# Optimization experiments

Hardware: AMD Instinct MI355X
Metric: run time of the kernel (lower is better)

## Reference

```python
import jax, jax.numpy as jnp
import numpy as np

N_NODES = 10000
N_EDGES = 320000
OBS_DIM = 30
ACT_DIM = 4
HID = 128


def setup_inputs() -> dict:
    key = jax.random.key(0)
    ks = jax.random.split(key, 16)

    def lin(k, fan_in, fan_out):
        s = 1.0 / np.sqrt(fan_in)
        kw, kb = jax.random.split(k)
        w = jax.random.uniform(kw, (fan_in, fan_out), jnp.float32, -s, s)
        b = jax.random.uniform(kb, (fan_out,), jnp.float32, -s, s)
        return w, b

    obs = jax.random.normal(ks[0], (N_NODES, OBS_DIM), jnp.float32)
    action = jax.random.normal(ks[1], (N_NODES, ACT_DIM), jnp.float32)
    edge_index = jax.random.randint(ks[2], (2, N_EDGES), 0, N_NODES, jnp.int64)

    w_g1, b_g1 = lin(ks[3], OBS_DIM + ACT_DIM, HID)
    w_g2, b_g2 = lin(ks[4], HID, HID)
    w_q1a, b_q1a = lin(ks[5], HID, HID)
    w_q1b, b_q1b = lin(ks[6], HID, 1)
    w_q2a, b_q2a = lin(ks[7], HID, HID)
    w_q2b, b_q2b = lin(ks[8], HID, 1)

    return dict(obs=obs, action=action, edge_index=edge_index,
                w_g1=w_g1, b_g1=b_g1, w_g2=w_g2, b_g2=b_g2,
                w_q1a=w_q1a, b_q1a=b_q1a, w_q1b=w_q1b, b_q1b=b_q1b,
                w_q2a=w_q2a, b_q2a=b_q2a, w_q2b=w_q2b, b_q2b=b_q2b)


def gcn_conv(x, w, b, src, dst, deg_inv_sqrt, n):
    xw = x @ w                                      # [N, Fout] small GEMM
    norm = deg_inv_sqrt[src] * deg_inv_sqrt[dst]    # [E'] edge norm
    msg = xw[src] * norm[:, None]                   # gather + scale, [E', Fout]
    out = jax.ops.segment_sum(msg, dst, num_segments=n)  # scatter-add
    return out + b


def reference(obs, action, edge_index,
              w_g1, b_g1, w_g2, b_g2,
              w_q1a, b_q1a, w_q1b, b_q1b,
              w_q2a, b_q2a, w_q2b, b_q2b):
    n = obs.shape[0]
    loops = jnp.arange(n, dtype=edge_index.dtype)
    src = jnp.concatenate([edge_index[0], loops])   # add self-loops
    dst = jnp.concatenate([edge_index[1], loops])

    deg = jnp.zeros((n,), jnp.float32).at[dst].add(1.0)
    deg_inv_sqrt = jnp.where(deg > 0, jax.lax.rsqrt(jnp.maximum(deg, 1.0)), 0.0)

    x = jnp.concatenate([obs, action], axis=1)
    x = jax.nn.relu(gcn_conv(x, w_g1, b_g1, src, dst, deg_inv_sqrt, n))
    x = jax.nn.relu(gcn_conv(x, w_g2, b_g2, src, dst, deg_inv_sqrt, n))

    q1 = jax.nn.relu(x @ w_q1a + b_q1a) @ w_q1b + b_q1b
    q2 = jax.nn.relu(x @ w_q2a + b_q2a) @ w_q2b + b_q2b
    return (q1, q2)
```

## Files before the change

### kernel.cpp

```cpp
#include <hip/hip_runtime.h>

#define N_NODES 10000
#define N_EDGES 320000
#define OBS_DIM 30
#define ACT_DIM 4
#define HID 128
#define ELL_W 128
#define SENT N_NODES


__global__ __launch_bounds__(256) void k_init(int* __restrict__ cnt,
                                              int* __restrict__ col,
                                              float* __restrict__ xpad,
                                              float* __restrict__ ph1,
                                              const float* __restrict__ obs,
                                              const float* __restrict__ act) {
    int i = blockIdx.x * 256 + threadIdx.x;
    if (i < N_NODES * ELL_W / 4)
        ((int4*)col)[i] = make_int4(SENT, SENT, SENT, SENT);
    if (i < (N_NODES + 1) * 16) {
        int row = i >> 4, sub = i & 15;
        float4 v = make_float4(0.f, 0.f, 0.f, 0.f);
        if (row < N_NODES) {
            float* vv = &v.x;
#pragma unroll
            for (int k = 0; k < 4; ++k) {
                int c = sub * 4 + k;
                if (c < OBS_DIM) vv[k] = obs[row * OBS_DIM + c];
                else if (c < OBS_DIM + ACT_DIM) vv[k] = act[row * ACT_DIM + (c - OBS_DIM)];
            }
        }
        ((float4*)xpad)[i] = v;
    }
    if (i <= N_NODES) cnt[i] = 0;
    if (i < HID / 4)
        ((float4*)(ph1 + (size_t)SENT * HID))[i] = make_float4(0.f, 0.f, 0.f, 0.f);
}


__global__ __launch_bounds__(256) void k_build(const int4* __restrict__ src4,
                                               const int4* __restrict__ dst4,
                                               int* __restrict__ cnt,
                                               int* __restrict__ col) {
    int i = blockIdx.x * 256 + threadIdx.x;
    if (i < N_EDGES / 4) {
        int4 s = src4[i];
        int4 d = dst4[i];
        int p;
        p = atomicAdd(&cnt[d.x], 1); col[(d.x << 7) + p] = s.x;
        p = atomicAdd(&cnt[d.y], 1); col[(d.y << 7) + p] = s.y;
        p = atomicAdd(&cnt[d.z], 1); col[(d.z << 7) + p] = s.z;
        p = atomicAdd(&cnt[d.w], 1); col[(d.w << 7) + p] = s.w;
    }
}


__global__ __launch_bounds__(512) void k_l1(const float4* __restrict__ x4,
                                            const int* __restrict__ cnt,
                                            const int* __restrict__ col,
                                            const float* __restrict__ W1,
                                            const float* __restrict__ b1,
                                            float* __restrict__ ph1) {
    __shared__ float w1s[34 * 128];
    __shared__ float zs[8][64];
    int t = threadIdx.x;
    {
        float4* wsp = (float4*)w1s;
        const float4* Wp = (const float4*)W1;
        for (int i = t; i < 1088; i += 512) wsp[i] = Wp[i];
    }
    __syncthreads();
    int wave = t >> 6, lane = t & 63, g = lane >> 4, sub = lane & 15;
    int node = blockIdx.x * 8 + wave;
    int deg = cnt[node];
    float di = rsqrtf((float)(deg + 1));
    const int* cp = col + (node << 7);
    float4 a = make_float4(0.f, 0.f, 0.f, 0.f);
    float4 b = make_float4(0.f, 0.f, 0.f, 0.f);
    if (g == 0) {
        float4 xv = x4[node * 16 + sub];
        a.x = di * xv.x; a.y = di * xv.y; a.z = di * xv.z; a.w = di * xv.w;
    }
    for (int e = 0; e < deg; e += 16) {
        int j0 = cp[e + g];
        int j1 = cp[e + 4 + g];
        int j2 = cp[e + 8 + g];
        int j3 = cp[e + 12 + g];
        float d0 = rsqrtf((float)(cnt[j0] + 1));
        float d1 = rsqrtf((float)(cnt[j1] + 1));
        float d2 = rsqrtf((float)(cnt[j2] + 1));
        float d3 = rsqrtf((float)(cnt[j3] + 1));
        float4 v0 = x4[j0 * 16 + sub];
        float4 v1 = x4[j1 * 16 + sub];
        float4 v2 = x4[j2 * 16 + sub];
        float4 v3 = x4[j3 * 16 + sub];
        a.x += d0 * v0.x + d1 * v1.x;
        a.y += d0 * v0.y + d1 * v1.y;
        a.z += d0 * v0.z + d1 * v1.z;
        a.w += d0 * v0.w + d1 * v1.w;
        b.x += d2 * v2.x + d3 * v3.x;
        b.y += d2 * v2.y + d3 * v3.y;
        b.z += d2 * v2.z + d3 * v3.z;
        b.w += d2 * v2.w + d3 * v3.w;
    }
    a.x += b.x; a.y += b.y; a.z += b.z; a.w += b.w;
    a.x += __shfl_xor(a.x, 16); a.x += __shfl_xor(a.x, 32);
    a.y += __shfl_xor(a.y, 16); a.y += __shfl_xor(a.y, 32);
    a.z += __shfl_xor(a.z, 16); a.z += __shfl_xor(a.z, 32);
    a.w += __shfl_xor(a.w, 16); a.w += __shfl_xor(a.w, 32);
    if (g == 0) {
        float4 z;
        z.x = di * a.x; z.y = di * a.y; z.z = di * a.z; z.w = di * a.w;
        *(float4*)&zs[wave][sub * 4] = z;
    }
    float h0 = b1[lane], h64 = b1[lane + 64];
#pragma unroll
    for (int k = 0; k < 34; ++k) {
        float zk = zs[wave][k];
        h0 += zk * w1s[k * 128 + lane];
        h64 += zk * w1s[k * 128 + 64 + lane];
    }
    ph1[node * HID + lane] = di * fmaxf(h0, 0.0f);
    ph1[node * HID + 64 + lane] = di * fmaxf(h64, 0.0f);
}


__global__ __launch_bounds__(256) void k_agg2(const float4* __restrict__ ph14,
                                              const int* __restrict__ cnt,
                                              const int* __restrict__ col,
                                              float4* __restrict__ sbuf) {
    int t = threadIdx.x;
    int wave = t >> 6, lane = t & 63, half = lane >> 5, sub = lane & 31;
    int node = blockIdx.x * 4 + wave;
    int deg = cnt[node];
    const int* cp = col + (node << 7);
    float4 a = make_float4(0.f, 0.f, 0.f, 0.f);
    float4 b = make_float4(0.f, 0.f, 0.f, 0.f);
    if (!half) a = ph14[node * 32 + sub];
    for (int e = 0; e < deg; e += 32) {
        int jj[16];
#pragma unroll
        for (int u = 0; u < 16; ++u) jj[u] = cp[e + 2 * u + half];
        float4 v[16];
#pragma unroll
        for (int u = 0; u < 16; ++u) v[u] = ph14[jj[u] * 32 + sub];
#pragma unroll
        for (int u = 0; u < 8; ++u) {
            a.x += v[u].x; a.y += v[u].y; a.z += v[u].z; a.w += v[u].w;
            b.x += v[u + 8].x; b.y += v[u + 8].y; b.z += v[u + 8].z; b.w += v[u + 8].w;
        }
    }
    a.x += b.x; a.y += b.y; a.z += b.z; a.w += b.w;
    a.x += __shfl_xor(a.x, 32);
    a.y += __shfl_xor(a.y, 32);
    a.z += __shfl_xor(a.z, 32);
    a.w += __shfl_xor(a.w, 32);
    if (!half) sbuf[node * 32 + sub] = a;
}


__global__ __launch_bounds__(256) void k_h2heads(const float4* __restrict__ sbuf4,
                                                 const int* __restrict__ cnt,
                                                 const float* __restrict__ W2, const float* __restrict__ b2,
                                                 const float* __restrict__ Wq1, const float* __restrict__ Bq1,
                                                 const float* __restrict__ w1b, const float* __restrict__ b1b,
                                                 const float* __restrict__ Wq2, const float* __restrict__ Bq2,
                                                 const float* __restrict__ w2b, const float* __restrict__ b2b,
                                                 float* __restrict__ q1, float* __restrict__ q2) {
    __shared__ float xs[16 * 128];
    __shared__ float hs[16 * 128];
    __shared__ float wbA[32 * 128];
    __shared__ float wbB[32 * 128];
    int t = threadIdx.x;
    int row0 = blockIdx.x * 16;
    {
        float4* xsp = (float4*)xs;
        for (int i = t; i < 512; i += 256) xsp[i] = sbuf4[row0 * 32 + i];
    }
    int lane = t & 63, wave = t >> 6;
    int c2 = lane * 2;
    int r0 = wave * 4;
    float2 acc[4];
#pragma unroll
    for (int r = 0; r < 4; ++r) acc[r] = make_float2(0.f, 0.f);
    for (int ch = 0; ch < 4; ++ch) {
        __syncthreads();
        {
            float4* wp = (float4*)wbA;
            const float4* Wp = (const float4*)(W2 + ch * 4096);
            for (int i = t; i < 1024; i += 256) wp[i] = Wp[i];
        }
        __syncthreads();
        for (int k4 = 0; k4 < 8; ++k4) {
            float4 xr[4];
#pragma unroll
            for (int r = 0; r < 4; ++r)
                xr[r] = *(const float4*)&xs[(r0 + r) * 128 + ch * 32 + k4 * 4];
#pragma unroll
            for (int j = 0; j < 4; ++j) {
                float2 w = *(const float2*)&wbA[(k4 * 4 + j) * 128 + c2];
#pragma unroll
                for (int r = 0; r < 4; ++r) {
                    float xv = (&xr[r].x)[j];
                    acc[r].x += xv * w.x;
                    acc[r].y += xv * w.y;
                }
            }
        }
    }
    {
        float bbx = b2[c2], bby = b2[c2 + 1];
#pragma unroll
        for (int r = 0; r < 4; ++r) {
            int row = row0 + r0 + r;
            float dr = rsqrtf((float)(cnt[row] + 1));
            hs[(r0 + r) * 128 + c2]     = fmaxf(dr * acc[r].x + bbx, 0.f);
            hs[(r0 + r) * 128 + c2 + 1] = fmaxf(dr * acc[r].y + bby, 0.f);
        }
    }
    float2 a1[4], a2[4];
#pragma unroll
    for (int r = 0; r < 4; ++r) {
        a1[r] = make_float2(0.f, 0.f);
        a2[r] = make_float2(0.f, 0.f);
    }
    for (int ch = 0; ch < 4; ++ch) {
        __syncthreads();
        {
            float4* w1p = (float4*)wbA;
            float4* w2p = (float4*)wbB;
            const float4* W1p = (const float4*)(Wq1 + ch * 4096);
            const float4* W2p = (const float4*)(Wq2 + ch * 4096);
            for (int i = t; i < 1024; i += 256) {
                w1p[i] = W1p[i];
                w2p[i] = W2p[i];
            }
        }
        __syncthreads();
        for (int k4 = 0; k4 < 8; ++k4) {
            float4 xr[4];
#pragma unroll
            for (int r = 0; r < 4; ++r)
                xr[r] = *(const float4*)&hs[(r0 + r) * 128 + ch * 32 + k4 * 4];
#pragma unroll
            for (int j = 0; j < 4; ++j) {
                float2 wA = *(const float2*)&wbA[(k4 * 4 + j) * 128 + c2];
                float2 wB = *(const float2*)&wbB[(k4 * 4 + j) * 128 + c2];
#pragma unroll
                for (int r = 0; r < 4; ++r) {
                    float xv = (&xr[r].x)[j];
                    a1[r].x += xv * wA.x;
                    a1[r].y += xv * wA.y;
                    a2[r].x += xv * wB.x;
                    a2[r].y += xv * wB.y;
                }
            }
        }
    }
    float B1x = Bq1[c2], B1y = Bq1[c2 + 1];
    float B2x = Bq2[c2], B2y = Bq2[c2 + 1];
    float v1x = w1b[c2], v1y = w1b[c2 + 1];
    float v2x = w2b[c2], v2y = w2b[c2 + 1];
    float s1[4], s2[4];
#pragma unroll
    for (int r = 0; r < 4; ++r) {
        s1[r] = fmaxf(a1[r].x + B1x, 0.f) * v1x + fmaxf(a1[r].y + B1y, 0.f) * v1y;
        s2[r] = fmaxf(a2[r].x + B2x, 0.f) * v2x + fmaxf(a2[r].y + B2y, 0.f) * v2y;
    }
#pragma unroll
    for (int off = 1; off < 64; off <<= 1) {
#pragma unroll
        for (int r = 0; r < 4; ++r) {
            s1[r] += __shfl_xor(s1[r], off);
            s2[r] += __shfl_xor(s2[r], off);
        }
    }
    if (lane == 0) {
        float bq1 = b1b[0], bq2 = b2b[0];
#pragma unroll
        for (int r = 0; r < 4; ++r) {
            int row = row0 + r0 + r;
            q1[row] = s1[r] + bq1;
            q2[row] = s2[r] + bq2;
        }
    }
}

extern "C" void kernel_launch(void* const* d_in, const int* in_sizes, int n_in,
                              void* d_out, int out_size, void* d_ws, size_t ws_size,
                              hipStream_t stream) {
    (void)in_sizes; (void)n_in; (void)out_size; (void)ws_size;
    const float* obs  = (const float*)d_in[0];
    const float* act  = (const float*)d_in[1];
    const int*   ei   = (const int*)d_in[2];
    const int*   src  = ei;
    const int*   dst  = ei + N_EDGES;
    const float* w_g1 = (const float*)d_in[3];
    const float* b_g1 = (const float*)d_in[4];
    const float* w_g2 = (const float*)d_in[5];
    const float* b_g2 = (const float*)d_in[6];
    const float* w_q1a = (const float*)d_in[7];
    const float* b_q1a = (const float*)d_in[8];
    const float* w_q1b = (const float*)d_in[9];
    const float* b_q1b = (const float*)d_in[10];
    const float* w_q2a = (const float*)d_in[11];
    const float* b_q2a = (const float*)d_in[12];
    const float* w_q2b = (const float*)d_in[13];
    const float* b_q2b = (const float*)d_in[14];
    float* out = (float*)d_out;

    char* ws = (char*)d_ws;
    size_t off = 0;
    auto alloc = [&](size_t bytes) {
        void* p = ws + off;
        off = (off + bytes + 255) & ~(size_t)255;
        return p;
    };
    int*   cnt  = (int*)alloc((N_NODES + 1) * 4);
    int*   col  = (int*)alloc((size_t)N_NODES * ELL_W * 4);
    float* xpad = (float*)alloc((size_t)(N_NODES + 1) * 64 * 4);
    float* ph1  = (float*)alloc((size_t)(N_NODES + 1) * HID * 4);
    float* sbuf = (float*)alloc((size_t)N_NODES * HID * 4);

    k_init<<<(N_NODES * ELL_W / 4 + 255) / 256, 256, 0, stream>>>(
        cnt, col, xpad, ph1, obs, act);
    k_build<<<(N_EDGES / 4 + 255) / 256, 256, 0, stream>>>(
        (const int4*)src, (const int4*)dst, cnt, col);
    k_l1<<<1250, 512, 0, stream>>>((const float4*)xpad, cnt, col, w_g1, b_g1, ph1);
    k_agg2<<<2500, 256, 0, stream>>>((const float4*)ph1, cnt, col, (float4*)sbuf);
    k_h2heads<<<625, 256, 0, stream>>>((const float4*)sbuf, cnt,
                                       w_g2, b_g2,
                                       w_q1a, b_q1a, w_q1b, b_q1b,
                                       w_q2a, b_q2a, w_q2b, b_q2b,
                                       out, out + N_NODES);
}
```

Before: 87.37 us.

## Split K across two wave groups in the fused dense-heads kernel

The k_h2heads block grows from 256 to 512 threads. Each half of the waves handles half of the K dimension, and the partial sums are combined through shared memory. Whole 128x128 weight matrices are now loaded into one 64KB shared buffer, so the chunked per-32-row reloads go away, and the two Q heads are computed one after the other instead of together. The aim is more parallelism per block and fewer barriers per chunk. In exchange the kernel adds more shared memory per block, extra reduction syncs, and serialized head computation, all of which may lower occupancy.

```diff
diff --git a/kernel.cpp b/kernel.cpp
--- a/kernel.cpp
+++ b/kernel.cpp
@@ -159,7 +159,7 @@
 }
 
 
-__global__ __launch_bounds__(256) void k_h2heads(const float4* __restrict__ sbuf4,
+__global__ __launch_bounds__(512) void k_h2heads(const float4* __restrict__ sbuf4,
                                                  const int* __restrict__ cnt,
                                                  const float* __restrict__ W2, const float* __restrict__ b2,
                                                  const float* __restrict__ Wq1, const float* __restrict__ Bq1,
@@ -169,119 +169,164 @@
                                                  float* __restrict__ q1, float* __restrict__ q2) {
     __shared__ float xs[16 * 128];
     __shared__ float hs[16 * 128];
-    __shared__ float wbA[32 * 128];
-    __shared__ float wbB[32 * 128];
+    __shared__ float wb[128 * 128];
     int t = threadIdx.x;
     int row0 = blockIdx.x * 16;
+    int lane = t & 63, wave = t >> 6;
+    int kh = wave >> 2;
+    int wr = wave & 3;
+    int c2 = lane * 2;
+    int r0 = wr * 4;
+    int kbase = kh * 64;
     {
         float4* xsp = (float4*)xs;
-        for (int i = t; i < 512; i += 256) xsp[i] = sbuf4[row0 * 32 + i];
-    }
-    int lane = t & 63, wave = t >> 6;
-    int c2 = lane * 2;
-    int r0 = wave * 4;
+        for (int i = t; i < 512; i += 512) xsp[i] = sbuf4[row0 * 32 + i];
+        float4* wp = (float4*)wb;
+        const float4* Wp = (const float4*)W2;
+        for (int i = t; i < 4096; i += 512) wp[i] = Wp[i];
+    }
+    __syncthreads();
     float2 acc[4];
 #pragma unroll
     for (int r = 0; r < 4; ++r) acc[r] = make_float2(0.f, 0.f);
-    for (int ch = 0; ch < 4; ++ch) {
-        __syncthreads();
-        {
-            float4* wp = (float4*)wbA;
-            const float4* Wp = (const float4*)(W2 + ch * 4096);
-            for (int i = t; i < 1024; i += 256) wp[i] = Wp[i];
-        }
-        __syncthreads();
-        for (int k4 = 0; k4 < 8; ++k4) {
-            float4 xr[4];
-#pragma unroll
-            for (int r = 0; r < 4; ++r)
-                xr[r] = *(const float4*)&xs[(r0 + r) * 128 + ch * 32 + k4 * 4];
-#pragma unroll
-            for (int j = 0; j < 4; ++j) {
-                float2 w = *(const float2*)&wbA[(k4 * 4 + j) * 128 + c2];
-#pragma unroll
-                for (int r = 0; r < 4; ++r) {
-                    float xv = (&xr[r].x)[j];
-                    acc[r].x += xv * w.x;
-                    acc[r].y += xv * w.y;
-                }
+    for (int k4 = 0; k4 < 16; ++k4) {
+        int k = kbase + k4 * 4;
+        float4 xr[4];
+#pragma unroll
+        for (int r = 0; r < 4; ++r)
+            xr[r] = *(const float4*)&xs[(r0 + r) * 128 + k];
+#pragma unroll
+        for (int j = 0; j < 4; ++j) {
+            float2 w = *(const float2*)&wb[(k + j) * 128 + c2];
+#pragma unroll
+            for (int r = 0; r < 4; ++r) {
+                float xv = (&xr[r].x)[j];
+                acc[r].x += xv * w.x;
+                acc[r].y += xv * w.y;
             }
         }
     }
-    {
+    if (kh == 1) {
+#pragma unroll
+        for (int r = 0; r < 4; ++r)
+            *(float2*)&hs[(r0 + r) * 128 + c2] = acc[r];
+    }
+    __syncthreads();
+    if (kh == 0) {
         float bbx = b2[c2], bby = b2[c2 + 1];
 #pragma unroll
         for (int r = 0; r < 4; ++r) {
             int row = row0 + r0 + r;
             float dr = rsqrtf((float)(cnt[row] + 1));
-            hs[(r0 + r) * 128 + c2]     = fmaxf(dr * acc[r].x + bbx, 0.f);
-            hs[(r0 + r) * 128 + c2 + 1] = fmaxf(dr * acc[r].y + bby, 0.f);
-        }
-    }
-    float2 a1[4], a2[4];
-#pragma unroll
-    for (int r = 0; r < 4; ++r) {
-        a1[r] = make_float2(0.f, 0.f);
-        a2[r] = make_float2(0.f, 0.f);
-    }
-    for (int ch = 0; ch < 4; ++ch) {
-        __syncthreads();
-        {
-            float4* w1p = (float4*)wbA;
-            float4* w2p = (float4*)wbB;
-            const float4* W1p = (const float4*)(Wq1 + ch * 4096);
-            const float4* W2p = (const float4*)(Wq2 + ch * 4096);
-            for (int i = t; i < 1024; i += 256) {
-                w1p[i] = W1p[i];
-                w2p[i] = W2p[i];
+            float2 p = *(const float2*)&hs[(r0 + r) * 128 + c2];
+            hs[(r0 + r) * 128 + c2]     = fmaxf(dr * (acc[r].x + p.x) + bbx, 0.f);
+            hs[(r0 + r) * 128 + c2 + 1] = fmaxf(dr * (acc[r].y + p.y) + bby, 0.f);
+        }
+    }
+    {
+        float4* wp = (float4*)wb;
+        const float4* Wp = (const float4*)Wq1;
+        for (int i = t; i < 4096; i += 512) wp[i] = Wp[i];
+    }
+    __syncthreads();
+    float2 a1[4];
+#pragma unroll
+    for (int r = 0; r < 4; ++r) a1[r] = make_float2(0.f, 0.f);
+    for (int k4 = 0; k4 < 16; ++k4) {
+        int k = kbase + k4 * 4;
+        float4 xr[4];
+#pragma unroll
+        for (int r = 0; r < 4; ++r)
+            xr[r] = *(const float4*)&hs[(r0 + r) * 128 + k];
+#pragma unroll
+        for (int j = 0; j < 4; ++j) {
+            float2 w = *(const float2*)&wb[(k + j) * 128 + c2];
+#pragma unroll
+            for (int r = 0; r < 4; ++r) {
+                float xv = (&xr[r].x)[j];
+                a1[r].x += xv * w.x;
+                a1[r].y += xv * w.y;
             }
         }
-        __syncthreads();
-        for (int k4 = 0; k4 < 8; ++k4) {
-            float4 xr[4];
-#pragma unroll
-            for (int r = 0; r < 4; ++r)
-                xr[r] = *(const float4*)&hs[(r0 + r) * 128 + ch * 32 + k4 * 4];
-#pragma unroll
-            for (int j = 0; j < 4; ++j) {
-                float2 wA = *(const float2*)&wbA[(k4 * 4 + j) * 128 + c2];
-                float2 wB = *(const float2*)&wbB[(k4 * 4 + j) * 128 + c2];
-#pragma unroll
-                for (int r = 0; r < 4; ++r) {
-                    float xv = (&xr[r].x)[j];
-                    a1[r].x += xv * wA.x;
-                    a1[r].y += xv * wA.y;
-                    a2[r].x += xv * wB.x;
-                    a2[r].y += xv * wB.y;
-                }
+    }
+    if (kh == 1) {
+#pragma unroll
+        for (int r = 0; r < 4; ++r)
+            *(float2*)&xs[(r0 + r) * 128 + c2] = a1[r];
+    }
+    __syncthreads();
+    if (kh == 0) {
+        float B1x = Bq1[c2], B1y = Bq1[c2 + 1];
+        float v1x = w1b[c2], v1y = w1b[c2 + 1];
+        float s1[4];
+#pragma unroll
+        for (int r = 0; r < 4; ++r) {
+            float2 p = *(const float2*)&xs[(r0 + r) * 128 + c2];
+            s1[r] = fmaxf(a1[r].x + p.x + B1x, 0.f) * v1x
+                  + fmaxf(a1[r].y + p.y + B1y, 0.f) * v1y;
+        }
+#pragma unroll
+        for (int off = 1; off < 64; off <<= 1) {
+#pragma unroll
+            for (int r = 0; r < 4; ++r) s1[r] += __shfl_xor(s1[r], off);
+        }
+        if (lane == 0) {
+            float bq1 = b1b[0];
+#pragma unroll
+            for (int r = 0; r < 4; ++r) q1[row0 + r0 + r] = s1[r] + bq1;
+        }
+    }
+    {
+        float4* wp = (float4*)wb;
+        const float4* Wp = (const float4*)Wq2;
+        for (int i = t; i < 4096; i += 512) wp[i] = Wp[i];
+    }
+    __syncthreads();
+    float2 a2[4];
+#pragma unroll
+    for (int r = 0; r < 4; ++r) a2[r] = make_float2(0.f, 0.f);
+    for (int k4 = 0; k4 < 16; ++k4) {
+        int k = kbase + k4 * 4;
+        float4 xr[4];
+#pragma unroll
+        for (int r = 0; r < 4; ++r)
+            xr[r] = *(const float4*)&hs[(r0 + r) * 128 + k];
+#pragma unroll
+        for (int j = 0; j < 4; ++j) {
+            float2 w = *(const float2*)&wb[(k + j) * 128 + c2];
+#pragma unroll
+            for (int r = 0; r < 4; ++r) {
+                float xv = (&xr[r].x)[j];
+                a2[r].x += xv * w.x;
+                a2[r].y += xv * w.y;
             }
         }
     }
-    float B1x = Bq1[c2], B1y = Bq1[c2 + 1];
-    float B2x = Bq2[c2], B2y = Bq2[c2 + 1];
-    float v1x = w1b[c2], v1y = w1b[c2 + 1];
-    float v2x = w2b[c2], v2y = w2b[c2 + 1];
-    float s1[4], s2[4];
-#pragma unroll
-    for (int r = 0; r < 4; ++r) {
-        s1[r] = fmaxf(a1[r].x + B1x, 0.f) * v1x + fmaxf(a1[r].y + B1y, 0.f) * v1y;
-        s2[r] = fmaxf(a2[r].x + B2x, 0.f) * v2x + fmaxf(a2[r].y + B2y, 0.f) * v2y;
-    }
-#pragma unroll
-    for (int off = 1; off < 64; off <<= 1) {
+    if (kh == 1) {
+#pragma unroll
+        for (int r = 0; r < 4; ++r)
+            *(float2*)&xs[(r0 + r) * 128 + c2] = a2[r];
+    }
+    __syncthreads();
+    if (kh == 0) {
+        float B2x = Bq2[c2], B2y = Bq2[c2 + 1];
+        float v2x = w2b[c2], v2y = w2b[c2 + 1];
+        float s2[4];
 #pragma unroll
         for (int r = 0; r < 4; ++r) {
-            s1[r] += __shfl_xor(s1[r], off);
-            s2[r] += __shfl_xor(s2[r], off);
-        }
-    }
-    if (lane == 0) {
-        float bq1 = b1b[0], bq2 = b2b[0];
-#pragma unroll
-        for (int r = 0; r < 4; ++r) {
-            int row = row0 + r0 + r;
-            q1[row] = s1[r] + bq1;
-            q2[row] = s2[r] + bq2;
+            float2 p = *(const float2*)&xs[(r0 + r) * 128 + c2];
+            s2[r] = fmaxf(a2[r].x + p.x + B2x, 0.f) * v2x
+                  + fmaxf(a2[r].y + p.y + B2y, 0.f) * v2y;
+        }
+#pragma unroll
+        for (int off = 1; off < 64; off <<= 1) {
+#pragma unroll
+            for (int r = 0; r < 4; ++r) s2[r] += __shfl_xor(s2[r], off);
+        }
+        if (lane == 0) {
+            float bq2 = b2b[0];
+#pragma unroll
+            for (int r = 0; r < 4; ++r) q2[row0 + r0 + r] = s2[r] + bq2;
         }
     }
 }
@@ -328,7 +373,7 @@
         (const int4*)src, (const int4*)dst, cnt, col);
     k_l1<<<1250, 512, 0, stream>>>((const float4*)xpad, cnt, col, w_g1, b_g1, ph1);
     k_agg2<<<2500, 256, 0, stream>>>((const float4*)ph1, cnt, col, (float4*)sbuf);
-    k_h2heads<<<625, 256, 0, stream>>>((const float4*)sbuf, cnt,
+    k_h2heads<<<625, 512, 0, stream>>>((const float4*)sbuf, cnt,
                                        w_g2, b_g2,
                                        w_q1a, b_q1a, w_q1b, b_q1b,
                                        w_q2a, b_q2a, w_q2b, b_q2b,
```

New measurement: 88.74 us. No clear change (+1.6%).
